# Optimization experiments

Measured on AMD Instinct MI355X. Metric: run time of the kernel, lower is better.

The kernel has to match this reference:

```python
import jax, jax.numpy as jnp
import numpy as np
import math

B, S, D, H, DFF = 4, 2048, 1024, 16, 4096
DK = D // H
EPS = 1e-5

def setup_inputs() -> dict:
    key = jax.random.key(0)
    ks = jax.random.split(key, 16)
    s_d = 1.0 / math.sqrt(D)
    s_ff = 1.0 / math.sqrt(DFF)
    return {
        "x": jax.random.normal(ks[0], (B, S, D), jnp.float32),
        "wq": jax.random.uniform(ks[1], (D, D), jnp.float32, -s_d, s_d),
        "bq": jnp.zeros((D,), jnp.float32),
        "wk": jax.random.uniform(ks[2], (D, D), jnp.float32, -s_d, s_d),
        "bk": jnp.zeros((D,), jnp.float32),
        "wv": jax.random.uniform(ks[3], (D, D), jnp.float32, -s_d, s_d),
        "bv": jnp.zeros((D,), jnp.float32),
        "wo": jax.random.uniform(ks[4], (D, D), jnp.float32, -s_d, s_d),
        "bo": jnp.zeros((D,), jnp.float32),
        "w1": jax.random.uniform(ks[5], (DFF, D), jnp.float32, -s_d, s_d),
        "b1": jnp.zeros((DFF,), jnp.float32),
        "w2": jax.random.uniform(ks[6], (D, DFF), jnp.float32, -s_ff, s_ff),
        "b2": jnp.zeros((D,), jnp.float32),
        "ln1_g": jnp.ones((D,), jnp.float32),
        "ln1_b": jnp.zeros((D,), jnp.float32),
        "ln2_g": jnp.ones((D,), jnp.float32),
        "ln2_b": jnp.zeros((D,), jnp.float32),
    }

def _layernorm(x, g, b):
    mu = jnp.mean(x, axis=-1, keepdims=True)
    var = jnp.mean(jnp.square(x - mu), axis=-1, keepdims=True)
    return (x - mu) * jax.lax.rsqrt(var + EPS) * g + b

def reference(x, wq, bq, wk, bk, wv, bv, wo, bo, w1, b1, w2, b2, ln1_g, ln1_b, ln2_g, ln2_b):
    # Multi-head self-attention (dropout in eval mode -> identity).
    Q = (x @ wq.T + bq).reshape(B, S, H, DK).transpose(0, 2, 1, 3)  # (B,H,S,DK)
    K = (x @ wk.T + bk).reshape(B, S, H, DK).transpose(0, 2, 1, 3)
    V = (x @ wv.T + bv).reshape(B, S, H, DK).transpose(0, 2, 1, 3)
    scores = jnp.einsum('bhqd,bhkd->bhqk', Q, K) / math.sqrt(DK)  # (B,H,S,S)
    attn = jax.nn.softmax(scores, axis=-1)
    ctx = jnp.einsum('bhqk,bhkd->bhqd', attn, V)
    ctx = ctx.transpose(0, 2, 1, 3).reshape(B, S, D)
    attn_out = ctx @ wo.T + bo
    # SkipConnection: x + norm(sublayer)  (post-applied LayerNorm on sublayer output)
    x = x + _layernorm(attn_out, ln1_g, ln1_b)
    # FFN
    ff = jax.nn.relu(x @ w1.T + b1) @ w2.T + b2
    return x + _layernorm(ff, ln2_g, ln2_b)
```

## Files before the change

kernel.cpp:

```cpp
#include <hip/hip_runtime.h>
#include <hip/hip_bf16.h>
#include <stdint.h>


#define DI __device__ __forceinline__

typedef __attribute__((ext_vector_type(4))) float f32x4;
typedef __attribute__((ext_vector_type(16))) float f32x16;
typedef __attribute__((ext_vector_type(8))) short bf16x8;
typedef __attribute__((ext_vector_type(4))) short s16x4;

#define B_ 4
#define S_ 2048
#define D_ 1024
#define H_ 16
#define DK_ 64
#define DFF_ 4096
#define M_ 8192

DI float bf2f(short s) {
  union { unsigned u; float f; } v;
  v.u = ((unsigned)(unsigned short)s) << 16;
  return v.f;
}
DI short f2bf(float f) {
  union { float f; unsigned u; } v;
  v.f = f;
  unsigned r = v.u + 0x7FFFu + ((v.u >> 16) & 1u);
  return (short)(r >> 16);
}
DI unsigned pkbf(float lo, float hi) {
  unsigned r;
  asm("v_cvt_pk_bf16_f32 %0, %1, %2" : "=v"(r) : "v"(lo), "v"(hi));
  return r;
}
DI void plswap(unsigned& a, unsigned& b) {
  asm volatile("v_permlane32_swap_b32 %0, %1" : "+v"(a), "+v"(b));
}
DI float ex2(float x) {
  float r;
  asm("v_exp_f32 %0, %1" : "=v"(r) : "v"(x));
  return r;
}
DI float max3(float a, float b, float c) {
  float r;
  asm("v_max3_f32 %0, %1, %2, %3" : "=v"(r) : "v"(a), "v"(b), "v"(c));
  return r;
}

__global__ __launch_bounds__(256) void cvt_kernel(const float* __restrict__ in,
                                                  short* __restrict__ out, int n) {
  long i = ((long)blockIdx.x * blockDim.x + threadIdx.x) * 8;
  if (i >= n) return;
  f32x4 a = *(const f32x4*)(in + i);
  f32x4 b = *(const f32x4*)(in + i + 4);
  bf16x8 r;
  r[0] = f2bf(a[0]); r[1] = f2bf(a[1]); r[2] = f2bf(a[2]); r[3] = f2bf(a[3]);
  r[4] = f2bf(b[0]); r[5] = f2bf(b[1]); r[6] = f2bf(b[2]); r[7] = f2bf(b[3]);
  *(bf16x8*)(out + i) = r;
}

DI void gl_lds16(const void* g, void* l) {
  __builtin_amdgcn_global_load_lds(
      (const __attribute__((address_space(1))) unsigned int*)g,
      (__attribute__((address_space(3))) unsigned int*)l, 16, 0, 0);
}

#define VMCNT(N) asm volatile("s_waitcnt vmcnt(" #N ")" ::: "memory")
#define LGKM0                                          \
  asm volatile("s_waitcnt lgkmcnt(0)" ::: "memory");   \
  __builtin_amdgcn_sched_barrier(0)

template <int BN, int MODE>
__global__ __launch_bounds__(512, 2)
void gemm_qs(const short* __restrict__ A, const short* __restrict__ Bm,
             const float* __restrict__ bias0, const float* __restrict__ bias1,
             const float* __restrict__ bias2, short* __restrict__ C,
             int M, int N, int K,
             short* __restrict__ Qo, short* __restrict__ Ko, short* __restrict__ Vo) {
  constexpr int WR = (BN == 256 ? 2 : 4);
  constexpr int WC = 8 / WR;
  constexpr int WM = 256 / WR;
  constexpr int WN = BN / WC;
  constexpr int MF = WM / 16;
  constexpr int NFr = WN / 16;
  constexpr int MH = MF / 2;
  constexpr int ASLOT = 256 * 32;
  constexpr int BSLOT = BN * 32;

  __shared__ short As[4 * ASLOT];
  __shared__ short Bs[4 * BSLOT];

  const int t = threadIdx.x, w = t >> 6, l = t & 63;
  const int wm = (WR == 2 ? (w >> 2) : (w >> 1));
  const int wn = (WR == 2 ? (w & 3) : (w & 1));
  const int lr = l & 15, lk = l >> 4;

  const int gx = gridDim.x;
  const int nwg = gx * gridDim.y;
  const int orig = blockIdx.y * gx + blockIdx.x;
  const int lin = (orig & 7) * (nwg >> 3) + (orig >> 3);
  const int row0 = (lin / gx) * 256;
  const int col0 = (lin % gx) * BN;

  const int NT = K >> 5;

  const int r0 = t >> 2, s0 = (((t & 3) ^ ((r0 >> 1) & 3)) << 3);
  const int r1 = r0 + 128, s1 = (((t & 3) ^ ((r1 >> 1) & 3)) << 3);
  const short* Asrc0 = A + (long)(row0 + r0) * K + s0;
  const short* Asrc1 = A + (long)(row0 + r1) * K + s1;
  const short* Bsrc0 = Bm + (long)(col0 + r0) * K + s0;
  const short* Bsrc1 = Bm + (long)(col0 + r1) * K + s1;
  const int d0 = t * 8, d1 = (t + 512) * 8;

  auto stageA = [&](int kt) {
    const int ko = kt << 5;
    short* Ab = As + (kt & 3) * ASLOT;
    gl_lds16(Asrc0 + ko, Ab + d0);
    gl_lds16(Asrc1 + ko, Ab + d1);
  };
  auto stageB = [&](int kt) {
    const int ko = kt << 5;
    short* Bb = Bs + (kt & 3) * BSLOT;
    gl_lds16(Bsrc0 + ko, Bb + d0);
    if constexpr (BN == 256) gl_lds16(Bsrc1 + ko, Bb + d1);
  };

  f32x4 acc[MF][NFr] = {};

  stageA(0); stageB(0);
  stageA(1); stageB(1);
  stageA(2); stageB(2);

  for (int kt = 0; kt < NT; ++kt) {
    if (kt + 2 < NT) {
      if constexpr (BN == 256) VMCNT(8); else VMCNT(6);
    } else if (kt + 1 < NT) {
      if constexpr (BN == 256) VMCNT(4); else VMCNT(3);
    } else {
      VMCNT(0);
    }
    __builtin_amdgcn_s_barrier();

    const short* aw = As + (kt & 3) * ASLOT + wm * (WM * 32);
    const short* bw = Bs + (kt & 3) * BSLOT + wn * (WN * 32);

    bf16x8 afr[MH], bfr[NFr];
#pragma unroll
    for (int m = 0; m < MH; ++m) {
      const int rr = m * 16 + lr;
      afr[m] = *(const bf16x8*)(aw + rr * 32 + ((lk ^ ((rr >> 1) & 3)) << 3));
    }
#pragma unroll
    for (int n = 0; n < NFr; ++n) {
      const int rr = n * 16 + lr;
      bfr[n] = *(const bf16x8*)(bw + rr * 32 + ((lk ^ ((rr >> 1) & 3)) << 3));
    }
    if (kt + 3 < NT) stageA(kt + 3);
    __builtin_amdgcn_s_barrier();
    LGKM0;
    __builtin_amdgcn_s_setprio(1);
#pragma unroll
    for (int m = 0; m < MH; ++m)
#pragma unroll
      for (int n = 0; n < NFr; ++n)
        acc[m][n] =
            __builtin_amdgcn_mfma_f32_16x16x32_bf16(afr[m], bfr[n], acc[m][n], 0, 0, 0);
    __builtin_amdgcn_s_setprio(0);

    bf16x8 af2[MH];
#pragma unroll
    for (int m = 0; m < MH; ++m) {
      const int rr = (MH + m) * 16 + lr;
      af2[m] = *(const bf16x8*)(aw + rr * 32 + ((lk ^ ((rr >> 1) & 3)) << 3));
    }
    if (kt + 3 < NT) stageB(kt + 3);
    __builtin_amdgcn_s_barrier();
    LGKM0;
    __builtin_amdgcn_s_setprio(1);
#pragma unroll
    for (int m = 0; m < MH; ++m)
#pragma unroll
      for (int n = 0; n < NFr; ++n)
        acc[MH + m][n] =
            __builtin_amdgcn_mfma_f32_16x16x32_bf16(af2[m], bfr[n], acc[MH + m][n], 0, 0, 0);
    __builtin_amdgcn_s_setprio(0);
  }

  if (MODE == 2) {
    const int which = col0 >> 10;
#pragma unroll
    for (int m = 0; m < MF; ++m) {
#pragma unroll
      for (int n = 0; n < NFr; ++n) {
        const int r0e = row0 + wm * WM + m * 16 + lk * 4;
        const int c = col0 + wn * WN + n * 16 + lr;
        const int cc = c & 1023;
        const int h = cc >> 6, dk = cc & 63;
        const int bb = r0e >> 11, s = r0e & 2047;
        if (which == 2) {
          const float bias = bias2[cc];
          s16x4 v4;
#pragma unroll
          for (int j = 0; j < 4; ++j) v4[j] = f2bf(acc[m][n][j] + bias);
          *(s16x4*)(Vo + ((long)((bb * H_ + h) * DK_ + dk)) * S_ + s) = v4;
        } else {
          const float bias = (which == 0 ? bias0[cc] : bias1[cc]);
          const float sc = (which == 0 ? 0.1803368801f : 1.0f);
          short* dst = (which == 0 ? Qo : Ko);
#pragma unroll
          for (int j = 0; j < 4; ++j)
            dst[(((long)(bb * H_ + h) * S_) + s + j) * DK_ + dk] =
                f2bf((acc[m][n][j] + bias) * sc);
        }
      }
    }
  } else {
#pragma unroll
    for (int m = 0; m < MF; ++m) {
#pragma unroll
      for (int n = 0; n < NFr; ++n) {
#pragma unroll
        for (int j = 0; j < 4; ++j) {
          const int r = row0 + wm * WM + m * 16 + lk * 4 + j;
          const int c = col0 + wn * WN + n * 16 + lr;
          float v = acc[m][n][j] + bias0[c];
          if (MODE == 1) v = fmaxf(v, 0.0f);
          C[(long)r * N + c] = f2bf(v);
        }
      }
    }
  }
}

__global__ __launch_bounds__(512, 4)
void attn_kernel(const short* __restrict__ Q, const short* __restrict__ K,
                 const short* __restrict__ Vt, short* __restrict__ ctx) {
  __shared__ short Ks[2 * 4096];
  __shared__ short Vs[2 * 4096];
  const int t = threadIdx.x, w = t >> 6, l = t & 63;
  const int q31 = l & 31, hi = l >> 5;

  const int orig = blockIdx.y * gridDim.x + blockIdx.x;
  const int xcd = orig & 7, k7 = orig >> 3;
  const int bh = xcd * 8 + (k7 >> 3);
  const int q0 = (k7 & 7) * 256 + w * 32;
  const long base = (long)bh * S_ * DK_;

  bf16x8 qf[4];
  {
    const short* qp = Q + base + (long)(q0 + q31) * DK_ + hi * 8;
#pragma unroll
    for (int ks = 0; ks < 4; ++ks) qf[ks] = *(const bf16x8*)(qp + ks * 16);
  }

  f32x16 oa[2] = {};
  float mrun = -1e30f, lrun = 0.0f;

  const int trow = t >> 3;
  const int tcol = (((t & 7) ^ (trow & 7)) << 3);
  const short* Ksrc = K + base + (long)trow * DK_ + tcol;
  const short* Vsrc = Vt + base + (long)trow * S_ + tcol;

  auto stg = [&](int tile, int slot) {
    const int kb = slot * 4096;
    const int kvn = tile * 64;
    gl_lds16(Ksrc + (long)kvn * DK_, &Ks[kb + t * 8]);
    gl_lds16(Vsrc + kvn, &Vs[kb + t * 8]);
  };

  stg(0, 0);

  for (int tt = 0; tt < 32; ++tt) {
    VMCNT(0);
    __builtin_amdgcn_s_barrier();
    if (tt + 1 < 32) stg(tt + 1, (tt + 1) & 1);
    const int cb = (tt & 1) * 4096;

    f32x16 sacc[2] = {};
#pragma unroll
    for (int m = 0; m < 2; ++m) {
      const int row = m * 32 + q31;
      const int sw = row & 7;
#pragma unroll
      for (int ks = 0; ks < 4; ++ks) {
        bf16x8 kf = *(const bf16x8*)&Ks[cb + row * 64 + (((2 * ks + hi) ^ sw) << 3)];
        sacc[m] = __builtin_amdgcn_mfma_f32_32x32x16_bf16(kf, qf[ks], sacc[m], 0, 0, 0);
      }
    }

    float mx[8];
#pragma unroll
    for (int r = 0; r < 8; ++r)
      mx[r] = fmaxf(max3(sacc[0][r], sacc[0][r + 8], sacc[1][r]), sacc[1][r + 8]);
    float ma = max3(mx[0], mx[1], mx[2]);
    float mb = max3(mx[3], mx[4], mx[5]);
    float tm = fmaxf(max3(mx[6], mx[7], ma), mb);
    tm = fmaxf(tm, __shfl_xor(tm, 32, 64));

    if (!__all(tm <= mrun + 8.0f)) {
      const float mnew = fmaxf(mrun, tm);
      const float fac = ex2(mrun - mnew);
      lrun *= fac;
#pragma unroll
      for (int m = 0; m < 2; ++m)
#pragma unroll
        for (int r = 0; r < 16; ++r) oa[m][r] *= fac;
      mrun = mnew;
    }

#pragma unroll
    for (int m = 0; m < 2; ++m)
#pragma unroll
      for (int r = 0; r < 16; ++r) sacc[m][r] = ex2(sacc[m][r] - mrun);

    float sm[8];
#pragma unroll
    for (int r = 0; r < 8; ++r)
      sm[r] = (sacc[0][r] + sacc[0][r + 8]) + (sacc[1][r] + sacc[1][r + 8]);
    sm[0] += sm[4]; sm[1] += sm[5]; sm[2] += sm[6]; sm[3] += sm[7];
    float ps = (sm[0] + sm[1]) + (sm[2] + sm[3]);
    ps += __shfl_xor(ps, 32, 64);
    lrun += ps;

    bf16x8 pf[4];
#pragma unroll
    for (int m = 0; m < 2; ++m)
#pragma unroll
      for (int sb = 0; sb < 2; ++sb) {
        unsigned p0 = pkbf(sacc[m][8 * sb + 0], sacc[m][8 * sb + 1]);
        unsigned p1 = pkbf(sacc[m][8 * sb + 2], sacc[m][8 * sb + 3]);
        unsigned p2 = pkbf(sacc[m][8 * sb + 4], sacc[m][8 * sb + 5]);
        unsigned p3 = pkbf(sacc[m][8 * sb + 6], sacc[m][8 * sb + 7]);
        plswap(p0, p2);
        plswap(p1, p3);
        union { unsigned u[4]; bf16x8 v; } fb;
        fb.u[0] = p0; fb.u[1] = p1; fb.u[2] = p2; fb.u[3] = p3;
        pf[2 * m + sb] = fb.v;
      }

#pragma unroll
    for (int mt = 0; mt < 2; ++mt) {
      const int row = mt * 32 + q31;
      const int sw = row & 7;
#pragma unroll
      for (int s = 0; s < 4; ++s) {
        bf16x8 vf = *(const bf16x8*)&Vs[cb + row * 64 + (((2 * s + hi) ^ sw) << 3)];
        oa[mt] = __builtin_amdgcn_mfma_f32_32x32x16_bf16(vf, pf[s], oa[mt], 0, 0, 0);
      }
    }
  }

  const int bb2 = bh >> 4, h = bh & 15;
  const float rl = 1.0f / lrun;
  short* crow = ctx + ((long)(bb2 * S_ + q0 + q31)) * D_ + h * 64 + 4 * hi;
#pragma unroll
  for (int mt = 0; mt < 2; ++mt)
#pragma unroll
    for (int g = 0; g < 4; ++g) {
      s16x4 v4;
#pragma unroll
      for (int i = 0; i < 4; ++i) v4[i] = f2bf(oa[mt][4 * g + i] * rl);
      *(s16x4*)(crow + mt * 32 + g * 8) = v4;
    }
}

template <int RES_BF16, int OUT_BF16>
__global__ __launch_bounds__(256)
void add_ln(const void* __restrict__ resv, const short* __restrict__ a,
            const float* __restrict__ gam, const float* __restrict__ bet,
            void* __restrict__ outv) {
  const int row = blockIdx.x, t = threadIdx.x;
  const int w = t >> 6, l = t & 63;
  const long roff = (long)row * D_;
  const int c = t * 4;
  s16x4 av = *(const s16x4*)(a + roff + c);
  float v0 = bf2f(av[0]), v1 = bf2f(av[1]), v2 = bf2f(av[2]), v3 = bf2f(av[3]);
  float s = v0 + v1 + v2 + v3;
#pragma unroll
  for (int mask = 1; mask < 64; mask <<= 1) s += __shfl_xor(s, mask, 64);
  __shared__ float r1[4], r2[4];
  if (l == 0) r1[w] = s;
  __syncthreads();
  float mu = (r1[0] + r1[1] + r1[2] + r1[3]) * (1.0f / D_);
  float d0 = v0 - mu, d1 = v1 - mu, d2 = v2 - mu, d3 = v3 - mu;
  float sq = d0 * d0 + d1 * d1 + d2 * d2 + d3 * d3;
#pragma unroll
  for (int mask = 1; mask < 64; mask <<= 1) sq += __shfl_xor(sq, mask, 64);
  if (l == 0) r2[w] = sq;
  __syncthreads();
  float var = (r2[0] + r2[1] + r2[2] + r2[3]) * (1.0f / D_);
  float rs = rsqrtf(var + 1e-5f);
  float res0, res1, res2, res3;
  if (RES_BF16) {
    s16x4 rv = *(const s16x4*)((const short*)resv + roff + c);
    res0 = bf2f(rv[0]); res1 = bf2f(rv[1]); res2 = bf2f(rv[2]); res3 = bf2f(rv[3]);
  } else {
    f32x4 rv = *(const f32x4*)((const float*)resv + roff + c);
    res0 = rv[0]; res1 = rv[1]; res2 = rv[2]; res3 = rv[3];
  }
  float o0 = res0 + d0 * rs * gam[c + 0] + bet[c + 0];
  float o1 = res1 + d1 * rs * gam[c + 1] + bet[c + 1];
  float o2 = res2 + d2 * rs * gam[c + 2] + bet[c + 2];
  float o3 = res3 + d3 * rs * gam[c + 3] + bet[c + 3];
  if (OUT_BF16) {
    s16x4 ov;
    ov[0] = f2bf(o0); ov[1] = f2bf(o1); ov[2] = f2bf(o2); ov[3] = f2bf(o3);
    *(s16x4*)((short*)outv + roff + c) = ov;
  } else {
    f32x4 ov;
    ov[0] = o0; ov[1] = o1; ov[2] = o2; ov[3] = o3;
    *(f32x4*)((float*)outv + roff + c) = ov;
  }
}

extern "C" void kernel_launch(void* const* d_in, const int* in_sizes, int n_in,
                              void* d_out, int out_size, void* d_ws, size_t ws_size,
                              hipStream_t stream) {
  (void)in_sizes; (void)n_in; (void)out_size; (void)ws_size;
  const float* x   = (const float*)d_in[0];
  const float* wq  = (const float*)d_in[1];
  const float* bq  = (const float*)d_in[2];
  const float* wk  = (const float*)d_in[3];
  const float* bk  = (const float*)d_in[4];
  const float* wv  = (const float*)d_in[5];
  const float* bv  = (const float*)d_in[6];
  const float* wo  = (const float*)d_in[7];
  const float* bo  = (const float*)d_in[8];
  const float* w1  = (const float*)d_in[9];
  const float* b1  = (const float*)d_in[10];
  const float* w2  = (const float*)d_in[11];
  const float* b2  = (const float*)d_in[12];
  const float* g1  = (const float*)d_in[13];
  const float* be1 = (const float*)d_in[14];
  const float* g2  = (const float*)d_in[15];
  const float* be2 = (const float*)d_in[16];

  char* ws = (char*)d_ws;
  const long MB = 1 << 20;
  short* xb    = (short*)(ws + 0 * MB);
  short* wqkvb = (short*)(ws + 16 * MB);
  short* wob   = (short*)(ws + 22 * MB);
  short* w1b   = (short*)(ws + 24 * MB);
  short* w2b   = (short*)(ws + 32 * MB);
  short* Qb    = (short*)(ws + 40 * MB);
  short* Kb    = (short*)(ws + 56 * MB);
  short* Vtb   = (short*)(ws + 72 * MB);
  short* ctxb  = (short*)(ws + 88 * MB);
  short* aout  = (short*)(ws + 40 * MB);
  short* x1b   = (short*)(ws + 56 * MB);
  short* hid   = (short*)(ws + 88 * MB);
  short* ffb   = (short*)(ws + 72 * MB);

  auto cvt = [&](const float* in, short* out, long n) {
    cvt_kernel<<<dim3((unsigned)((n / 8 + 255) / 256)), dim3(256), 0, stream>>>(in, out, (int)n);
  };
  cvt(x, xb, (long)M_ * D_);
  cvt(wq, wqkvb + 0L * D_ * D_, (long)D_ * D_);
  cvt(wk, wqkvb + 1L * D_ * D_, (long)D_ * D_);
  cvt(wv, wqkvb + 2L * D_ * D_, (long)D_ * D_);
  cvt(wo, wob, (long)D_ * D_);
  cvt(w1, w1b, (long)DFF_ * D_);
  cvt(w2, w2b, (long)D_ * DFF_);

  gemm_qs<256, 2><<<dim3(3072 / 256, M_ / 256), 512, 0, stream>>>(
      xb, wqkvb, bq, bk, bv, nullptr, M_, 3072, D_, Qb, Kb, Vtb);

  attn_kernel<<<dim3(S_ / 256, B_ * H_), 512, 0, stream>>>(Qb, Kb, Vtb, ctxb);

  gemm_qs<128, 0><<<dim3(D_ / 128, M_ / 256), 512, 0, stream>>>(
      ctxb, wob, bo, nullptr, nullptr, aout, M_, D_, D_, nullptr, nullptr, nullptr);

  add_ln<0, 1><<<dim3(M_), 256, 0, stream>>>(x, aout, g1, be1, x1b);

  gemm_qs<256, 1><<<dim3(DFF_ / 256, M_ / 256), 512, 0, stream>>>(
      x1b, w1b, b1, nullptr, nullptr, hid, M_, DFF_, D_, nullptr, nullptr, nullptr);
  gemm_qs<128, 0><<<dim3(D_ / 128, M_ / 256), 512, 0, stream>>>(
      hid, w2b, b2, nullptr, nullptr, ffb, M_, D_, DFF_, nullptr, nullptr, nullptr);

  add_ln<1, 0><<<dim3(M_), 256, 0, stream>>>(x1b, ffb, g2, be2, d_out);
}
```

Measured before the change: 413.0 us.

## Restructure GEMM into 8-phase ping-pong pipeline with K=64 tiles

Replaces the GEMM mainloop with a double-buffered K=64 tile scheme split into four MFMA quadrant phases. Each phase interleaves LDS fragment loads and global-to-LDS staging of half-tiles with barriers and priority hints, so memory traffic overlaps compute more finely. It also changes the swizzle to an 8-way XOR layout and remaps workgroups to a 2D XCD-aware tile grid. The cost is more barriers per iteration and subtle buffer-reuse ordering that could race or add sync overhead.

```diff
diff --git a/kernel.cpp b/kernel.cpp
--- a/kernel.cpp
+++ b/kernel.cpp
@@ -70,121 +70,156 @@
 #define LGKM0                                          \
   asm volatile("s_waitcnt lgkmcnt(0)" ::: "memory");   \
   __builtin_amdgcn_sched_barrier(0)
+#define BAR __builtin_amdgcn_s_barrier()
+#define PRIO1 __builtin_amdgcn_s_setprio(1)
+#define PRIO0 __builtin_amdgcn_s_setprio(0)
+
+DI bf16x8 ldf(const short* base, int row, int kk, int lk) {
+  return *(const bf16x8*)(base + row * 64 + (((4 * kk + lk) ^ (row & 7)) << 3));
+}
 
 template <int BN, int MODE>
 __global__ __launch_bounds__(512, 2)
-void gemm_qs(const short* __restrict__ A, const short* __restrict__ Bm,
-             const float* __restrict__ bias0, const float* __restrict__ bias1,
-             const float* __restrict__ bias2, short* __restrict__ C,
-             int M, int N, int K,
-             short* __restrict__ Qo, short* __restrict__ Ko, short* __restrict__ Vo) {
-  constexpr int WR = (BN == 256 ? 2 : 4);
-  constexpr int WC = 8 / WR;
-  constexpr int WM = 256 / WR;
-  constexpr int WN = BN / WC;
-  constexpr int MF = WM / 16;
-  constexpr int NFr = WN / 16;
-  constexpr int MH = MF / 2;
-  constexpr int ASLOT = 256 * 32;
-  constexpr int BSLOT = BN * 32;
-
-  __shared__ short As[4 * ASLOT];
-  __shared__ short Bs[4 * BSLOT];
+void gemm8p(const short* __restrict__ A, const short* __restrict__ Bm,
+            const float* __restrict__ bias0, const float* __restrict__ bias1,
+            const float* __restrict__ bias2, short* __restrict__ C,
+            int M, int N, int K,
+            short* __restrict__ Qo, short* __restrict__ Ko, short* __restrict__ Vo) {
+  constexpr int BH = BN / 128;
+  constexpr int MQ = (BN == 256 ? 4 : 2);
+  constexpr int NQ = 2;
+  constexpr int MF = 2 * MQ;
+  constexpr int NFr = 4;
+  constexpr int WM = (BN == 256 ? 128 : 64);
+  constexpr int WN = 64;
+
+  __shared__ short As[2 * 2 * 8192];
+  __shared__ short Bs[2 * BH * 8192];
 
   const int t = threadIdx.x, w = t >> 6, l = t & 63;
-  const int wm = (WR == 2 ? (w >> 2) : (w >> 1));
-  const int wn = (WR == 2 ? (w & 3) : (w & 1));
+  const int wm = (BN == 256 ? (w >> 2) : (w >> 1));
+  const int wn = (BN == 256 ? (w & 3) : (w & 1));
   const int lr = l & 15, lk = l >> 4;
-
-  const int gx = gridDim.x;
-  const int nwg = gx * gridDim.y;
+  const int ah = (BN == 256 ? wm : (wm >> 1));
+  const int ab = (BN == 256 ? 0 : (wm & 1) * 64);
+  const int bh = (BN == 256 ? (wn >> 1) : 0);
+  const int bb = (BN == 256 ? (wn & 1) * 64 : wn * 64);
+
+  const int gx = gridDim.x, gy = gridDim.y;
   const int orig = blockIdx.y * gx + blockIdx.x;
-  const int lin = (orig & 7) * (nwg >> 3) + (orig >> 3);
-  const int row0 = (lin / gx) * 256;
-  const int col0 = (lin % gx) * BN;
-
-  const int NT = K >> 5;
-
-  const int r0 = t >> 2, s0 = (((t & 3) ^ ((r0 >> 1) & 3)) << 3);
-  const int r1 = r0 + 128, s1 = (((t & 3) ^ ((r1 >> 1) & 3)) << 3);
-  const short* Asrc0 = A + (long)(row0 + r0) * K + s0;
-  const short* Asrc1 = A + (long)(row0 + r1) * K + s1;
-  const short* Bsrc0 = Bm + (long)(col0 + r0) * K + s0;
-  const short* Bsrc1 = Bm + (long)(col0 + r1) * K + s1;
-  const int d0 = t * 8, d1 = (t + 512) * 8;
-
-  auto stageA = [&](int kt) {
-    const int ko = kt << 5;
-    short* Ab = As + (kt & 3) * ASLOT;
-    gl_lds16(Asrc0 + ko, Ab + d0);
-    gl_lds16(Asrc1 + ko, Ab + d1);
+  const int xcd = orig & 7, k7 = orig >> 3;
+  const int rw = gx >> 1, rh = gy >> 2;
+  const int row0 = ((xcd >> 1) * rh + k7 / rw) * 256;
+  const int col0 = ((xcd & 1) * rw + k7 % rw) * BN;
+
+  const int NT = K >> 6;
+
+  const int rl0 = t >> 3;
+  const int csw = ((t & 7) ^ (rl0 & 7)) << 3;
+  const short* Abase = A + (long)row0 * K;
+  const short* Bbase = Bm + (long)col0 * K;
+
+  auto stA = [&](int b, int kt, int h) {
+    short* dst = As + ((b * 2 + h) << 13);
+    const short* s = Abase + (long)(h * 128 + rl0) * K + (kt << 6) + csw;
+    gl_lds16(s, dst + t * 8);
+    gl_lds16(s + (long)64 * K, dst + (t + 512) * 8);
   };
-  auto stageB = [&](int kt) {
-    const int ko = kt << 5;
-    short* Bb = Bs + (kt & 3) * BSLOT;
-    gl_lds16(Bsrc0 + ko, Bb + d0);
-    if constexpr (BN == 256) gl_lds16(Bsrc1 + ko, Bb + d1);
+  auto stB = [&](int b, int kt, int h) {
+    short* dst = Bs + ((b * BH + h) << 13);
+    const short* s = Bbase + (long)(h * 128 + rl0) * K + (kt << 6) + csw;
+    gl_lds16(s, dst + t * 8);
+    gl_lds16(s + (long)64 * K, dst + (t + 512) * 8);
   };
 
   f32x4 acc[MF][NFr] = {};
 
-  stageA(0); stageB(0);
-  stageA(1); stageB(1);
-  stageA(2); stageB(2);
-
-  for (int kt = 0; kt < NT; ++kt) {
-    if (kt + 2 < NT) {
-      if constexpr (BN == 256) VMCNT(8); else VMCNT(6);
-    } else if (kt + 1 < NT) {
-      if constexpr (BN == 256) VMCNT(4); else VMCNT(3);
+  stA(0, 0, 0); stA(0, 0, 1);
+  stB(0, 0, 0); if (BH == 2) stB(0, 0, 1);
+  stB(1, 1, 0); if (BH == 2) stB(1, 1, 1);
+  stA(1, 1, 0);
+  if (BH == 2) { VMCNT(6); } else { VMCNT(4); }
+  BAR;
+
+  for (int u = 0; u < NT; ++u) {
+    const int rb = u & 1, ob = rb ^ 1;
+    const short* aw = As + ((rb * 2 + ah) << 13);
+    const short* bw = Bs + ((rb * BH + bh) << 13);
+    const bool m1 = (u + 1 < NT), m2 = (u + 2 < NT);
+    bf16x8 a0[MQ][2], a1[MQ][2], b0[NQ][2], b1[NQ][2];
+
+#pragma unroll
+    for (int m = 0; m < MQ; ++m) {
+      const int r = ab + m * 16 + lr;
+      a0[m][0] = ldf(aw, r, 0, lk); a0[m][1] = ldf(aw, r, 1, lk);
+    }
+#pragma unroll
+    for (int n = 0; n < NQ; ++n) {
+      const int r = bb + n * 16 + lr;
+      b0[n][0] = ldf(bw, r, 0, lk); b0[n][1] = ldf(bw, r, 1, lk);
+    }
+    if (m1) stA(ob, u + 1, 1);
+    BAR; LGKM0; PRIO1;
+#pragma unroll
+    for (int m = 0; m < MQ; ++m)
+#pragma unroll
+      for (int n = 0; n < NQ; ++n)
+#pragma unroll
+        for (int kk = 0; kk < 2; ++kk)
+          acc[m][n] = __builtin_amdgcn_mfma_f32_16x16x32_bf16(
+              a0[m][kk], b0[n][kk], acc[m][n], 0, 0, 0);
+    PRIO0; BAR;
+
+#pragma unroll
+    for (int n = 0; n < NQ; ++n) {
+      const int r = bb + (NQ + n) * 16 + lr;
+      b1[n][0] = ldf(bw, r, 0, lk); b1[n][1] = ldf(bw, r, 1, lk);
+    }
+    BAR; LGKM0; PRIO1;
+#pragma unroll
+    for (int m = 0; m < MQ; ++m)
+#pragma unroll
+      for (int n = 0; n < NQ; ++n)
+#pragma unroll
+        for (int kk = 0; kk < 2; ++kk)
+          acc[m][NQ + n] = __builtin_amdgcn_mfma_f32_16x16x32_bf16(
+              a0[m][kk], b1[n][kk], acc[m][NQ + n], 0, 0, 0);
+    PRIO0; BAR;
+
+#pragma unroll
+    for (int m = 0; m < MQ; ++m) {
+      const int r = ab + (MQ + m) * 16 + lr;
+      a1[m][0] = ldf(aw, r, 0, lk); a1[m][1] = ldf(aw, r, 1, lk);
+    }
+    if (m2) stB(rb, u + 2, 0);
+    BAR; LGKM0; PRIO1;
+#pragma unroll
+    for (int m = 0; m < MQ; ++m)
+#pragma unroll
+      for (int n = 0; n < NQ; ++n)
+#pragma unroll
+        for (int kk = 0; kk < 2; ++kk)
+          acc[MQ + m][NQ + n] = __builtin_amdgcn_mfma_f32_16x16x32_bf16(
+              a1[m][kk], b1[n][kk], acc[MQ + m][NQ + n], 0, 0, 0);
+    PRIO0; BAR;
+
+    if (m2) { if (BH == 2) stB(rb, u + 2, 1); stA(rb, u + 2, 0); }
+    BAR; PRIO1;
+#pragma unroll
+    for (int m = 0; m < MQ; ++m)
+#pragma unroll
+      for (int n = 0; n < NQ; ++n)
+#pragma unroll
+        for (int kk = 0; kk < 2; ++kk)
+          acc[MQ + m][n] = __builtin_amdgcn_mfma_f32_16x16x32_bf16(
+              a1[m][kk], b0[n][kk], acc[MQ + m][n], 0, 0, 0);
+    PRIO0;
+    if (m2) {
+      if (BH == 2) { VMCNT(6); } else { VMCNT(4); }
     } else {
       VMCNT(0);
     }
-    __builtin_amdgcn_s_barrier();
-
-    const short* aw = As + (kt & 3) * ASLOT + wm * (WM * 32);
-    const short* bw = Bs + (kt & 3) * BSLOT + wn * (WN * 32);
-
-    bf16x8 afr[MH], bfr[NFr];
-#pragma unroll
-    for (int m = 0; m < MH; ++m) {
-      const int rr = m * 16 + lr;
-      afr[m] = *(const bf16x8*)(aw + rr * 32 + ((lk ^ ((rr >> 1) & 3)) << 3));
-    }
-#pragma unroll
-    for (int n = 0; n < NFr; ++n) {
-      const int rr = n * 16 + lr;
-      bfr[n] = *(const bf16x8*)(bw + rr * 32 + ((lk ^ ((rr >> 1) & 3)) << 3));
-    }
-    if (kt + 3 < NT) stageA(kt + 3);
-    __builtin_amdgcn_s_barrier();
-    LGKM0;
-    __builtin_amdgcn_s_setprio(1);
-#pragma unroll
-    for (int m = 0; m < MH; ++m)
-#pragma unroll
-      for (int n = 0; n < NFr; ++n)
-        acc[m][n] =
-            __builtin_amdgcn_mfma_f32_16x16x32_bf16(afr[m], bfr[n], acc[m][n], 0, 0, 0);
-    __builtin_amdgcn_s_setprio(0);
-
-    bf16x8 af2[MH];
-#pragma unroll
-    for (int m = 0; m < MH; ++m) {
-      const int rr = (MH + m) * 16 + lr;
-      af2[m] = *(const bf16x8*)(aw + rr * 32 + ((lk ^ ((rr >> 1) & 3)) << 3));
-    }
-    if (kt + 3 < NT) stageB(kt + 3);
-    __builtin_amdgcn_s_barrier();
-    LGKM0;
-    __builtin_amdgcn_s_setprio(1);
-#pragma unroll
-    for (int m = 0; m < MH; ++m)
-#pragma unroll
-      for (int n = 0; n < NFr; ++n)
-        acc[MH + m][n] =
-            __builtin_amdgcn_mfma_f32_16x16x32_bf16(af2[m], bfr[n], acc[MH + m][n], 0, 0, 0);
-    __builtin_amdgcn_s_setprio(0);
+    BAR;
   }
 
   if (MODE == 2) {
@@ -197,20 +232,20 @@
         const int c = col0 + wn * WN + n * 16 + lr;
         const int cc = c & 1023;
         const int h = cc >> 6, dk = cc & 63;
-        const int bb = r0e >> 11, s = r0e & 2047;
+        const int bbx = r0e >> 11, s = r0e & 2047;
         if (which == 2) {
           const float bias = bias2[cc];
           s16x4 v4;
 #pragma unroll
           for (int j = 0; j < 4; ++j) v4[j] = f2bf(acc[m][n][j] + bias);
-          *(s16x4*)(Vo + ((long)((bb * H_ + h) * DK_ + dk)) * S_ + s) = v4;
+          *(s16x4*)(Vo + ((long)((bbx * H_ + h) * DK_ + dk)) * S_ + s) = v4;
         } else {
           const float bias = (which == 0 ? bias0[cc] : bias1[cc]);
           const float sc = (which == 0 ? 0.1803368801f : 1.0f);
           short* dst = (which == 0 ? Qo : Ko);
 #pragma unroll
           for (int j = 0; j < 4; ++j)
-            dst[(((long)(bb * H_ + h) * S_) + s + j) * DK_ + dk] =
+            dst[(((long)(bbx * H_ + h) * S_) + s + j) * DK_ + dk] =
                 f2bf((acc[m][n][j] + bias) * sc);
         }
       }
@@ -273,7 +308,7 @@
 
   for (int tt = 0; tt < 32; ++tt) {
     VMCNT(0);
-    __builtin_amdgcn_s_barrier();
+    BAR;
     if (tt + 1 < 32) stg(tt + 1, (tt + 1) & 1);
     const int cb = (tt & 1) * 4096;
 
@@ -463,19 +498,19 @@
   cvt(w1, w1b, (long)DFF_ * D_);
   cvt(w2, w2b, (long)D_ * DFF_);
 
-  gemm_qs<256, 2><<<dim3(3072 / 256, M_ / 256), 512, 0, stream>>>(
+  gemm8p<256, 2><<<dim3(3072 / 256, M_ / 256), 512, 0, stream>>>(
       xb, wqkvb, bq, bk, bv, nullptr, M_, 3072, D_, Qb, Kb, Vtb);
 
   attn_kernel<<<dim3(S_ / 256, B_ * H_), 512, 0, stream>>>(Qb, Kb, Vtb, ctxb);
 
-  gemm_qs<128, 0><<<dim3(D_ / 128, M_ / 256), 512, 0, stream>>>(
+  gemm8p<128, 0><<<dim3(D_ / 128, M_ / 256), 512, 0, stream>>>(
       ctxb, wob, bo, nullptr, nullptr, aout, M_, D_, D_, nullptr, nullptr, nullptr);
 
   add_ln<0, 1><<<dim3(M_), 256, 0, stream>>>(x, aout, g1, be1, x1b);
 
-  gemm_qs<256, 1><<<dim3(DFF_ / 256, M_ / 256), 512, 0, stream>>>(
+  gemm8p<256, 1><<<dim3(DFF_ / 256, M_ / 256), 512, 0, stream>>>(
       x1b, w1b, b1, nullptr, nullptr, hid, M_, DFF_, D_, nullptr, nullptr, nullptr);
-  gemm_qs<128, 0><<<dim3(D_ / 128, M_ / 256), 512, 0, stream>>>(
+  gemm8p<128, 0><<<dim3(D_ / 128, M_ / 256), 512, 0, stream>>>(
       hid, w2b, b2, nullptr, nullptr, ffb, M_, D_, DFF_, nullptr, nullptr, nullptr);
 
   add_ln<1, 0><<<dim3(M_), 256, 0, stream>>>(x1b, ffb, g2, be2, d_out);
```

Result: faster. 385.6 us (-6.6%).
